# Kernel optimization log

Hardware: AMD Instinct MI355X
Metric: run time of the kernel (lower is better)

Reference implementation:

```python
import jax, jax.numpy as jnp
import numpy as np

N_NODES = 100000
N_EDGES = 3200000
IN_CH = 512
HIDDEN = 64
LOC_OUT = 16
OUT_CH = 40


def setup_inputs() -> dict:
    key = jax.random.key(0)
    ks = jax.random.split(key, 10)
    return {
        "batch_x": jax.random.normal(ks[0], (N_NODES, IN_CH), dtype=jnp.float32),
        "edge_index": jax.random.randint(ks[1], (2, N_EDGES), 0, N_NODES, dtype=jnp.int64),
        "glob_emb": jax.random.normal(ks[2], (N_NODES, LOC_OUT), dtype=jnp.float32),
        "W1": jax.random.normal(ks[3], (IN_CH, HIDDEN), dtype=jnp.float32) * (1.0 / np.sqrt(IN_CH)),
        "b1": jnp.zeros((HIDDEN,), dtype=jnp.float32),
        "W2": jax.random.normal(ks[4], (HIDDEN, LOC_OUT), dtype=jnp.float32) * (1.0 / np.sqrt(HIDDEN)),
        "b2": jnp.zeros((LOC_OUT,), dtype=jnp.float32),
        "att_w1": jax.random.normal(ks[5], (LOC_OUT, 16), dtype=jnp.float32) * 0.25,
        "att_b1": jnp.zeros((16,), dtype=jnp.float32),
        "att_w2": jax.random.normal(ks[6], (16, 1), dtype=jnp.float32) * 0.25,
        "lin1_w": jax.random.normal(ks[7], (LOC_OUT, OUT_CH), dtype=jnp.float32) * 0.25,
        "lin1_b": jnp.zeros((OUT_CH,), dtype=jnp.float32),
    }


def _gcn_conv(x, W, b, row, col, n):
    # GCNConv: out = D^-1/2 (A + I) D^-1/2 (X W) + b   (PyG default: self-loops, sym norm)
    h = x @ W
    loops = jnp.arange(n, dtype=row.dtype)
    row2 = jnp.concatenate([row, loops])  # sources (x_j)
    col2 = jnp.concatenate([col, loops])  # targets (aggregation index)
    deg = jax.ops.segment_sum(jnp.ones_like(col2, dtype=h.dtype), col2, num_segments=n)
    dinv = jax.lax.rsqrt(jnp.maximum(deg, 1.0))  # deg >= 1 thanks to self-loops
    norm = dinv[row2] * dinv[col2]               # [E+N]
    agg = jax.ops.segment_sum(h[row2] * norm[:, None], col2, num_segments=n)
    return agg + b


def reference(batch_x, edge_index, glob_emb, W1, b1, W2, b2, att_w1, att_b1, att_w2, lin1_w, lin1_b):
    n = batch_x.shape[0]
    row, col = edge_index[0], edge_index[1]
    x = _gcn_conv(batch_x, W1, b1, row, col, n)
    x = jax.nn.relu(x)  # dropout p=0.0 -> identity
    x = _gcn_conv(x, W2, b2, row, col, n)  # last layer: no relu/dropout
    z = jnp.stack([x, glob_emb], axis=1)  # [N, 2, 16]
    w = jnp.tanh(z @ att_w1 + att_b1) @ att_w2  # [N, 2, 1]
    beta = jax.nn.softmax(w, axis=1)
    emb = jnp.sum(beta * z, axis=1)  # [N, 16]
    return emb @ lin1_w + lin1_b  # [N, 40]
```

## Files before the change

kernel.cpp:

```cpp
#include <hip/hip_runtime.h>

#define N_IN 512
#define HID 64
#define NBLK 256

typedef __attribute__((ext_vector_type(4))) float f32x4;
typedef __attribute__((ext_vector_type(8))) short bf16x8;

__device__ inline float bf2f(unsigned short s) {
    union { unsigned int u; float f; } v; v.u = ((unsigned int)s) << 16; return v.f;
}
__device__ inline unsigned short f2bf(float f) {
    union { float f; unsigned int u; } v; v.f = f;
    unsigned int u = v.u;
    return (unsigned short)((u + 0x7FFFu + ((u >> 16) & 1u)) >> 16);
}

__global__ __launch_bounds__(1024) void k_histA_wt(const int* __restrict__ EI, int* __restrict__ hist,
                                                   const float* __restrict__ W1, unsigned short* __restrict__ Wt,
                                                   int E, int N, int K) {
    int tid = threadIdx.x;
    if (blockIdx.x >= NBLK) {
        int i = (blockIdx.x - NBLK) * 1024 + tid;
        if (i < N_IN * HID) {
            int k = i >> 6, n = i & 63;
            Wt[n * 512 + k] = f2bf(W1[i]);
        }
        return;
    }
    __shared__ int hs[512];
    __shared__ int sflag;
    if (tid == 0) sflag = (EI[1] == 0 && EI[3] == 0 && EI[5] == 0 && EI[7] == 0) ? 1 : 0;
    if (tid < 512) hs[tid] = 0;
    __syncthreads();
    bool f = sflag != 0;
    int chunk = (E + NBLK - 1) / NBLK;
    int s = blockIdx.x * chunk, e = min(E, s + chunk);
    for (int i = s + tid; i < e; i += 1024) {
        int c = f ? ((const int2*)EI)[E + i].x : EI[E + i];
        if ((unsigned)c < (unsigned)N) atomicAdd(&hs[c >> 8], 1);
    }
    __syncthreads();
    for (int k = tid; k < K; k += 1024) hist[k * NBLK + blockIdx.x] = hs[k];
}

__global__ __launch_bounds__(256) void k_scan_a2(int* __restrict__ data, int* __restrict__ bsum, int n) {
    __shared__ int sd[256];
    int i = blockIdx.x * 256 + threadIdx.x;
    int v = (i < n) ? data[i] : 0;
    sd[threadIdx.x] = v;
    __syncthreads();
    for (int off = 1; off < 256; off <<= 1) {
        int t = 0;
        if (threadIdx.x >= (unsigned)off) t = sd[threadIdx.x - off];
        __syncthreads();
        sd[threadIdx.x] += t;
        __syncthreads();
    }
    if (i < n) data[i] = sd[threadIdx.x] - v;
    if (threadIdx.x == 255) bsum[blockIdx.x] = sd[255];
}

__global__ __launch_bounds__(512) void k_scan_b(const int* __restrict__ bsum, int* __restrict__ bexc, int nb) {
    __shared__ int sd[512];
    int t = threadIdx.x;
    int v = (t < nb) ? bsum[t] : 0;
    sd[t] = v;
    __syncthreads();
    for (int off = 1; off < 512; off <<= 1) {
        int u = 0;
        if (t >= off) u = sd[t - off];
        __syncthreads();
        sd[t] += u;
        __syncthreads();
    }
    if (t < nb) bexc[t] = sd[t] - v;
    if (t == 511) bexc[nb] = sd[511];
}

__global__ __launch_bounds__(1024) void k_partB(const int* __restrict__ EI, const int* __restrict__ hist,
                                                const int* __restrict__ bexc, int* __restrict__ edges2,
                                                int E, int N, int K) {
    __shared__ int cur[512];
    __shared__ int sflag;
    int tid = threadIdx.x, b = blockIdx.x;
    if (tid == 0) sflag = (EI[1] == 0 && EI[3] == 0 && EI[5] == 0 && EI[7] == 0) ? 1 : 0;
    if (tid < 512) cur[tid] = (tid < K) ? (bexc[tid] + hist[tid * NBLK + b]) : 0;
    __syncthreads();
    bool f = sflag != 0;
    int chunk = (E + NBLK - 1) / NBLK;
    int s = b * chunk, e = min(E, s + chunk);
    for (int i = s + tid; i < e; i += 1024) {
        int r, c;
        if (f) { const int2* E2 = (const int2*)EI; r = E2[i].x; c = E2[E + i].x; }
        else   { r = EI[i]; c = EI[E + i]; }
        if ((unsigned)r >= (unsigned)N || (unsigned)c >= (unsigned)N) continue;
        int pos = atomicAdd(&cur[c >> 8], 1);
        edges2[pos] = r | ((c & 255) << 20);
    }
}

__global__ __launch_bounds__(256) void k_gemm1(const float* __restrict__ X, const unsigned short* __restrict__ Wt,
                                               unsigned short* __restrict__ H, int N) {
    int tid = threadIdx.x;
    int w = tid >> 6, lane = tid & 63;
    int m_l = lane & 15, q = lane >> 4;
    int m0 = blockIdx.x * 128 + w * 32;
    int rA0 = m0 + m_l, rA1 = m0 + 16 + m_l;
    int rc0 = rA0 < N ? rA0 : N - 1;
    int rc1 = rA1 < N ? rA1 : N - 1;
    const float* baseA0 = X + (size_t)rc0 * 512 + q * 8;
    const float* baseA1 = X + (size_t)rc1 * 512 + q * 8;
    const unsigned short* baseB = Wt + (size_t)m_l * 512 + q * 8;

    f32x4 acc[2][4] = {};
#pragma unroll 4
    for (int c = 0; c < 16; ++c) {
        int ko = c * 32;
        float4 x0a = *(const float4*)(baseA0 + ko);
        float4 x0b = *(const float4*)(baseA0 + ko + 4);
        float4 x1a = *(const float4*)(baseA1 + ko);
        float4 x1b = *(const float4*)(baseA1 + ko + 4);
        bf16x8 a0, a1;
        a0[0] = (short)f2bf(x0a.x); a0[1] = (short)f2bf(x0a.y); a0[2] = (short)f2bf(x0a.z); a0[3] = (short)f2bf(x0a.w);
        a0[4] = (short)f2bf(x0b.x); a0[5] = (short)f2bf(x0b.y); a0[6] = (short)f2bf(x0b.z); a0[7] = (short)f2bf(x0b.w);
        a1[0] = (short)f2bf(x1a.x); a1[1] = (short)f2bf(x1a.y); a1[2] = (short)f2bf(x1a.z); a1[3] = (short)f2bf(x1a.w);
        a1[4] = (short)f2bf(x1b.x); a1[5] = (short)f2bf(x1b.y); a1[6] = (short)f2bf(x1b.z); a1[7] = (short)f2bf(x1b.w);
#pragma unroll
        for (int t = 0; t < 4; ++t) {
            bf16x8 bb = *(const bf16x8*)(baseB + (size_t)t * 16 * 512 + ko);
            acc[0][t] = __builtin_amdgcn_mfma_f32_16x16x32_bf16(a0, bb, acc[0][t], 0, 0, 0);
            acc[1][t] = __builtin_amdgcn_mfma_f32_16x16x32_bf16(a1, bb, acc[1][t], 0, 0, 0);
        }
    }
#pragma unroll
    for (int h = 0; h < 2; ++h) {
#pragma unroll
        for (int rg = 0; rg < 4; ++rg) {
            int row = m0 + h * 16 + q * 4 + rg;
            if (row < N) {
#pragma unroll
                for (int t = 0; t < 4; ++t)
                    H[(size_t)row * 64 + t * 16 + m_l] = f2bf(acc[h][t][rg]);
            }
        }
    }
}

__global__ __launch_bounds__(256) void k_bucket(const int* __restrict__ bexc, const int* __restrict__ edges2,
                                                int* __restrict__ edges, int* __restrict__ start,
                                                float* __restrict__ dinv, unsigned short* __restrict__ H,
                                                int N, int K) {
    __shared__ int hist[256], sd[256], cur[256];
    __shared__ float dvs[256];
    int b = blockIdx.x, tid = threadIdx.x;
    int base = bexc[b];
    int end  = bexc[b + 1];
    hist[tid] = 0;
    __syncthreads();
    for (int i = base + tid; i < end; i += 256)
        atomicAdd(&hist[(edges2[i] >> 20) & 255], 1);
    __syncthreads();
    int v = hist[tid];
    sd[tid] = v;
    __syncthreads();
    for (int off = 1; off < 256; off <<= 1) {
        int t = 0;
        if (tid >= off) t = sd[tid - off];
        __syncthreads();
        sd[tid] += t;
        __syncthreads();
    }
    int excl = sd[tid] - v;
    cur[tid] = excl;
    int node = b * 256 + tid;
    float dvv = rsqrtf((float)(v + 1));
    dvs[tid] = dvv;
    if (node < N) {
        start[node] = base + excl;
        dinv[node] = dvv;
    }
    if (b == 0 && tid == 0) start[N] = bexc[K];
    __syncthreads();
    for (int i = base + tid; i < end; i += 256) {
        int pv = edges2[i];
        int pos = atomicAdd(&cur[(pv >> 20) & 255], 1);
        edges[base + pos] = pv & 0xFFFFF;
    }
    for (int rr = tid >> 4; rr < 256; rr += 16) {
        int n2 = b * 256 + rr;
        if (n2 < N) {
            float dv2 = dvs[rr];
            uint2* pp = (uint2*)(H + (size_t)n2 * 64 + (size_t)(tid & 15) * 4);
            uint2 vv = *pp;
            float f0 = bf2f((unsigned short)(vv.x & 0xffffu)) * dv2;
            float f1 = bf2f((unsigned short)(vv.x >> 16)) * dv2;
            float f2 = bf2f((unsigned short)(vv.y & 0xffffu)) * dv2;
            float f3 = bf2f((unsigned short)(vv.y >> 16)) * dv2;
            vv.x = (unsigned int)f2bf(f0) | ((unsigned int)f2bf(f1) << 16);
            vv.y = (unsigned int)f2bf(f2) | ((unsigned int)f2bf(f3) << 16);
            *pp = vv;
        }
    }
}

__global__ __launch_bounds__(256) void k_agg1g2(const unsigned short* __restrict__ H, const int* __restrict__ edges,
                                                const int* __restrict__ start, const float* __restrict__ dinv,
                                                const float* __restrict__ b1, const float* __restrict__ W2,
                                                unsigned short* __restrict__ H2, int N) {
    __shared__ float w2s[64 * 17];
    int tid = threadIdx.x;
    for (int i = tid; i < 1024; i += 256) { int k = i >> 4, c = i & 15; w2s[k * 17 + c] = W2[i]; }
    __syncthreads();
    int wid = blockIdx.x * 4 + (tid >> 6);
    int lane = tid & 63;
    if (wid >= N) return;
    int g = lane >> 4;
    int c4 = lane & 15;
    const size_t coff = (size_t)c4 * 4;
    float a0 = 0.f, a1 = 0.f, a2 = 0.f, a3 = 0.f;
    int s = start[wid], e = start[wid + 1];
    int i = s;
    if ((i & 3) && i < e) {
        int lim = min(e, (i + 3) & ~3);
        int j = i + g;
        if (j < lim) {
            uint2 v = *(const uint2*)(H + (size_t)edges[j] * 64 + coff);
            a0 += __uint_as_float(v.x << 16);
            a1 += __uint_as_float(v.x & 0xffff0000u);
            a2 += __uint_as_float(v.y << 16);
            a3 += __uint_as_float(v.y & 0xffff0000u);
        }
        i = lim;
    }
    for (; i + 32 <= e; i += 32) {
        int4 s0 = *(const int4*)(edges + i + g * 4);
        int4 s1 = *(const int4*)(edges + i + 16 + g * 4);
        uint2 v0 = *(const uint2*)(H + (size_t)s0.x * 64 + coff);
        uint2 v1 = *(const uint2*)(H + (size_t)s0.y * 64 + coff);
        uint2 v2 = *(const uint2*)(H + (size_t)s0.z * 64 + coff);
        uint2 v3 = *(const uint2*)(H + (size_t)s0.w * 64 + coff);
        uint2 v4 = *(const uint2*)(H + (size_t)s1.x * 64 + coff);
        uint2 v5 = *(const uint2*)(H + (size_t)s1.y * 64 + coff);
        uint2 v6 = *(const uint2*)(H + (size_t)s1.z * 64 + coff);
        uint2 v7 = *(const uint2*)(H + (size_t)s1.w * 64 + coff);
        a0 += __uint_as_float(v0.x << 16) + __uint_as_float(v1.x << 16)
            + __uint_as_float(v2.x << 16) + __uint_as_float(v3.x << 16)
            + __uint_as_float(v4.x << 16) + __uint_as_float(v5.x << 16)
            + __uint_as_float(v6.x << 16) + __uint_as_float(v7.x << 16);
        a1 += __uint_as_float(v0.x & 0xffff0000u) + __uint_as_float(v1.x & 0xffff0000u)
            + __uint_as_float(v2.x & 0xffff0000u) + __uint_as_float(v3.x & 0xffff0000u)
            + __uint_as_float(v4.x & 0xffff0000u) + __uint_as_float(v5.x & 0xffff0000u)
            + __uint_as_float(v6.x & 0xffff0000u) + __uint_as_float(v7.x & 0xffff0000u);
        a2 += __uint_as_float(v0.y << 16) + __uint_as_float(v1.y << 16)
            + __uint_as_float(v2.y << 16) + __uint_as_float(v3.y << 16)
            + __uint_as_float(v4.y << 16) + __uint_as_float(v5.y << 16)
            + __uint_as_float(v6.y << 16) + __uint_as_float(v7.y << 16);
        a3 += __uint_as_float(v0.y & 0xffff0000u) + __uint_as_float(v1.y & 0xffff0000u)
            + __uint_as_float(v2.y & 0xffff0000u) + __uint_as_float(v3.y & 0xffff0000u)
            + __uint_as_float(v4.y & 0xffff0000u) + __uint_as_float(v5.y & 0xffff0000u)
            + __uint_as_float(v6.y & 0xffff0000u) + __uint_as_float(v7.y & 0xffff0000u);
    }
    if (i + 16 <= e) {
        int4 sv = *(const int4*)(edges + i + g * 4);
        uint2 v0 = *(const uint2*)(H + (size_t)sv.x * 64 + coff);
        uint2 v1 = *(const uint2*)(H + (size_t)sv.y * 64 + coff);
        uint2 v2 = *(const uint2*)(H + (size_t)sv.z * 64 + coff);
        uint2 v3 = *(const uint2*)(H + (size_t)sv.w * 64 + coff);
        a0 += __uint_as_float(v0.x << 16) + __uint_as_float(v1.x << 16)
            + __uint_as_float(v2.x << 16) + __uint_as_float(v3.x << 16);
        a1 += __uint_as_float(v0.x & 0xffff0000u) + __uint_as_float(v1.x & 0xffff0000u)
            + __uint_as_float(v2.x & 0xffff0000u) + __uint_as_float(v3.x & 0xffff0000u);
        a2 += __uint_as_float(v0.y << 16) + __uint_as_float(v1.y << 16)
            + __uint_as_float(v2.y << 16) + __uint_as_float(v3.y << 16);
        a3 += __uint_as_float(v0.y & 0xffff0000u) + __uint_as_float(v1.y & 0xffff0000u)
            + __uint_as_float(v2.y & 0xffff0000u) + __uint_as_float(v3.y & 0xffff0000u);
        i += 16;
    }
    for (; i < e; i += 4) {
        int j = i + g;
        if (j < e) {
            uint2 v = *(const uint2*)(H + (size_t)edges[j] * 64 + coff);
            a0 += __uint_as_float(v.x << 16);
            a1 += __uint_as_float(v.x & 0xffff0000u);
            a2 += __uint_as_float(v.y << 16);
            a3 += __uint_as_float(v.y & 0xffff0000u);
        }
    }
    a0 += __shfl_xor(a0, 16, 64); a0 += __shfl_xor(a0, 32, 64);
    a1 += __shfl_xor(a1, 16, 64); a1 += __shfl_xor(a1, 32, 64);
    a2 += __shfl_xor(a2, 16, 64); a2 += __shfl_xor(a2, 32, 64);
    a3 += __shfl_xor(a3, 16, 64); a3 += __shfl_xor(a3, 32, 64);
    float dv = dinv[wid];
    uint2 sv = *(const uint2*)(H + (size_t)wid * 64 + coff);
    a0 += __uint_as_float(sv.x << 16);
    a1 += __uint_as_float(sv.x & 0xffff0000u);
    a2 += __uint_as_float(sv.y << 16);
    a3 += __uint_as_float(sv.y & 0xffff0000u);
    float4 bv = *(const float4*)(b1 + c4 * 4);
    float r0 = fmaxf(a0 * dv + bv.x, 0.f);
    float r1 = fmaxf(a1 * dv + bv.y, 0.f);
    float r2 = fmaxf(a2 * dv + bv.z, 0.f);
    float r3 = fmaxf(a3 * dv + bv.w, 0.f);
    float p = 0.f;
#pragma unroll
    for (int j = 0; j < 4; ++j) {
        int src = 4 * g + j;
        float x0 = __shfl(r0, src, 64);
        float x1 = __shfl(r1, src, 64);
        float x2 = __shfl(r2, src, 64);
        float x3 = __shfl(r3, src, 64);
        int kb = 16 * g + 4 * j;
        p += x0 * w2s[(kb + 0) * 17 + c4];
        p += x1 * w2s[(kb + 1) * 17 + c4];
        p += x2 * w2s[(kb + 2) * 17 + c4];
        p += x3 * w2s[(kb + 3) * 17 + c4];
    }
    p += __shfl_xor(p, 16, 64);
    p += __shfl_xor(p, 32, 64);
    if (g == 0) H2[(size_t)wid * 16 + c4] = f2bf(p * dv);
}

__global__ __launch_bounds__(256) void k_agg2(const unsigned short* __restrict__ H2, const int* __restrict__ edges,
                                              const int* __restrict__ start, const float* __restrict__ dinv,
                                              const float* __restrict__ b2, float* __restrict__ X2, int N) {
    int wid = blockIdx.x * 4 + (threadIdx.x >> 6);
    int lane = threadIdx.x & 63;
    if (wid >= N) return;
    int g = lane >> 3;
    int c2 = lane & 7;
    const size_t coff = (size_t)c2 * 2;
    float a0 = 0.f, a1 = 0.f;
    int s = start[wid], e = start[wid + 1];
    int i = s;
    if ((i & 3) && i < e) {
        int lim = min(e, (i + 3) & ~3);
        int j = i + g;
        if (j < lim) {
            unsigned int v = *(const unsigned int*)(H2 + (size_t)edges[j] * 16 + coff);
            a0 += __uint_as_float(v << 16);
            a1 += __uint_as_float(v & 0xffff0000u);
        }
        i = lim;
    }
    for (; i + 64 <= e; i += 64) {
        int4 s0 = *(const int4*)(edges + i + g * 4);
        int4 s1 = *(const int4*)(edges + i + 32 + g * 4);
        unsigned int v0 = *(const unsigned int*)(H2 + (size_t)s0.x * 16 + coff);
        unsigned int v1 = *(const unsigned int*)(H2 + (size_t)s0.y * 16 + coff);
        unsigned int v2 = *(const unsigned int*)(H2 + (size_t)s0.z * 16 + coff);
        unsigned int v3 = *(const unsigned int*)(H2 + (size_t)s0.w * 16 + coff);
        unsigned int v4 = *(const unsigned int*)(H2 + (size_t)s1.x * 16 + coff);
        unsigned int v5 = *(const unsigned int*)(H2 + (size_t)s1.y * 16 + coff);
        unsigned int v6 = *(const unsigned int*)(H2 + (size_t)s1.z * 16 + coff);
        unsigned int v7 = *(const unsigned int*)(H2 + (size_t)s1.w * 16 + coff);
        a0 += __uint_as_float(v0 << 16) + __uint_as_float(v1 << 16)
            + __uint_as_float(v2 << 16) + __uint_as_float(v3 << 16)
            + __uint_as_float(v4 << 16) + __uint_as_float(v5 << 16)
            + __uint_as_float(v6 << 16) + __uint_as_float(v7 << 16);
        a1 += __uint_as_float(v0 & 0xffff0000u) + __uint_as_float(v1 & 0xffff0000u)
            + __uint_as_float(v2 & 0xffff0000u) + __uint_as_float(v3 & 0xffff0000u)
            + __uint_as_float(v4 & 0xffff0000u) + __uint_as_float(v5 & 0xffff0000u)
            + __uint_as_float(v6 & 0xffff0000u) + __uint_as_float(v7 & 0xffff0000u);
    }
    if (i + 32 <= e) {
        int4 sv = *(const int4*)(edges + i + g * 4);
        unsigned int v0 = *(const unsigned int*)(H2 + (size_t)sv.x * 16 + coff);
        unsigned int v1 = *(const unsigned int*)(H2 + (size_t)sv.y * 16 + coff);
        unsigned int v2 = *(const unsigned int*)(H2 + (size_t)sv.z * 16 + coff);
        unsigned int v3 = *(const unsigned int*)(H2 + (size_t)sv.w * 16 + coff);
        a0 += __uint_as_float(v0 << 16) + __uint_as_float(v1 << 16)
            + __uint_as_float(v2 << 16) + __uint_as_float(v3 << 16);
        a1 += __uint_as_float(v0 & 0xffff0000u) + __uint_as_float(v1 & 0xffff0000u)
            + __uint_as_float(v2 & 0xffff0000u) + __uint_as_float(v3 & 0xffff0000u);
        i += 32;
    }
    for (; i < e; i += 8) {
        int j = i + g;
        if (j < e) {
            unsigned int v = *(const unsigned int*)(H2 + (size_t)edges[j] * 16 + coff);
            a0 += __uint_as_float(v << 16);
            a1 += __uint_as_float(v & 0xffff0000u);
        }
    }
    a0 += __shfl_xor(a0, 8, 64); a0 += __shfl_xor(a0, 16, 64); a0 += __shfl_xor(a0, 32, 64);
    a1 += __shfl_xor(a1, 8, 64); a1 += __shfl_xor(a1, 16, 64); a1 += __shfl_xor(a1, 32, 64);
    if (g == 0) {
        float dv = dinv[wid];
        unsigned int sv = *(const unsigned int*)(H2 + (size_t)wid * 16 + coff);
        a0 += __uint_as_float(sv << 16);
        a1 += __uint_as_float(sv & 0xffff0000u);
        float2 bv = *(const float2*)(b2 + c2 * 2);
        float2 o; o.x = a0 * dv + bv.x; o.y = a1 * dv + bv.y;
        *(float2*)(X2 + (size_t)wid * 16 + coff) = o;
    }
}

__global__ __launch_bounds__(256) void k_head(const float* __restrict__ X2, const float* __restrict__ G,
                                              const float* __restrict__ AW1, const float* __restrict__ AB1,
                                              const float* __restrict__ AW2, const float* __restrict__ LW,
                                              const float* __restrict__ LB, float* __restrict__ OUT, int N) {
    __shared__ float s_aw1[256], s_ab1[16], s_aw2[16], s_lw[640], s_lb[40];
    int tid = threadIdx.x;
    s_aw1[tid] = AW1[tid];
    if (tid < 16) { s_ab1[tid] = AB1[tid]; s_aw2[tid] = AW2[tid]; }
    for (int i = tid; i < 640; i += 256) s_lw[i] = LW[i];
    if (tid < 40) s_lb[tid] = LB[tid];
    __syncthreads();
    int node = blockIdx.x * 256 + tid;
    if (node >= N) return;
    float x[16], g[16];
    const float4* xp = (const float4*)(X2 + (size_t)node * 16);
    const float4* gp = (const float4*)(G + (size_t)node * 16);
#pragma unroll
    for (int q = 0; q < 4; ++q) {
        float4 v = xp[q]; x[q*4] = v.x; x[q*4+1] = v.y; x[q*4+2] = v.z; x[q*4+3] = v.w;
        float4 u = gp[q]; g[q*4] = u.x; g[q*4+1] = u.y; g[q*4+2] = u.z; g[q*4+3] = u.w;
    }
    float wx = 0.f, wg = 0.f;
#pragma unroll
    for (int j = 0; j < 16; ++j) {
        float tx = s_ab1[j], tg = s_ab1[j];
#pragma unroll
        for (int c = 0; c < 16; ++c) { tx += x[c] * s_aw1[c*16 + j]; tg += g[c] * s_aw1[c*16 + j]; }
        wx += tanhf(tx) * s_aw2[j];
        wg += tanhf(tg) * s_aw2[j];
    }
    float m = fmaxf(wx, wg);
    float ex = expf(wx - m), eg = expf(wg - m);
    float inv = 1.f / (ex + eg);
    float bx = ex * inv, bg = eg * inv;
    float emb[16];
#pragma unroll
    for (int c = 0; c < 16; ++c) emb[c] = bx * x[c] + bg * g[c];
    float* op = OUT + (size_t)node * 40;
    for (int o = 0; o < 40; ++o) {
        float a = s_lb[o];
#pragma unroll
        for (int c = 0; c < 16; ++c) a += emb[c] * s_lw[c*40 + o];
        op[o] = a;
    }
}

extern "C" void kernel_launch(void* const* d_in, const int* in_sizes, int n_in,
                              void* d_out, int out_size, void* d_ws, size_t ws_size,
                              hipStream_t stream) {
    const float* X   = (const float*)d_in[0];
    const int*   EI  = (const int*)d_in[1];
    const float* G   = (const float*)d_in[2];
    const float* W1  = (const float*)d_in[3];
    const float* B1  = (const float*)d_in[4];
    const float* W2  = (const float*)d_in[5];
    const float* B2  = (const float*)d_in[6];
    const float* AW1 = (const float*)d_in[7];
    const float* AB1 = (const float*)d_in[8];
    const float* AW2 = (const float*)d_in[9];
    const float* LW  = (const float*)d_in[10];
    const float* LB  = (const float*)d_in[11];
    float* OUT = (float*)d_out;

    const int N = in_sizes[0] / N_IN;
    const int E = in_sizes[1] / 2;
    const int NB = (N + 255) / 256;
    const int K  = NB;
    const int NH = K * NBLK;
    const int SB = (NH + 255) / 256;
    const int WB = (N_IN * HID + 1023) / 1024;
    const int GB = (N + 127) / 128;

    char* w = (char*)d_ws;
    size_t off = 0;
    auto take = [&](size_t bytes) -> void* {
        void* p = (void*)(w + off);
        off = (off + bytes + 255) & ~(size_t)255;
        return p;
    };
    int*   hist   = (int*)take((size_t)NH * 4);
    int*   bsum   = (int*)take((size_t)SB * 4);
    int*   bexc   = (int*)take((size_t)(SB + 1) * 4);
    int*   startp = (int*)take((size_t)(N + 1) * 4);
    float* dinvp  = (float*)take((size_t)N * 4);
    int*   edges2 = (int*)take((size_t)E * 4);
    int*   edges  = (int*)take((size_t)E * 4);
    unsigned short* wt = (unsigned short*)take((size_t)N_IN * HID * 2);
    unsigned short* h1 = (unsigned short*)take((size_t)N * 64 * 2);
    unsigned short* h2 = (unsigned short*)take((size_t)N * 16 * 2);
    float* x2 = (float*)take((size_t)N * 16 * 4);
    (void)ws_size; (void)n_in; (void)out_size;

    k_histA_wt<<<NBLK + WB, 1024, 0, stream>>>(EI, hist, W1, wt, E, N, K);
    k_scan_a2 <<<SB, 256, 0, stream>>>(hist, bsum, NH);
    k_scan_b  <<<1, 512, 0, stream>>>(bsum, bexc, SB);
    k_partB   <<<NBLK, 1024, 0, stream>>>(EI, hist, bexc, edges2, E, N, K);
    k_gemm1   <<<GB, 256, 0, stream>>>(X, wt, h1, N);
    k_bucket  <<<K, 256, 0, stream>>>(bexc, edges2, edges, startp, dinvp, h1, N, K);
    k_agg1g2  <<<(N + 3) / 4, 256, 0, stream>>>(h1, edges, startp, dinvp, B1, W2, h2, N);
    k_agg2    <<<(N + 3) / 4, 256, 0, stream>>>(h2, edges, startp, dinvp, B2, x2, N);
    k_head    <<<NB, 256, 0, stream>>>(x2, G, AW1, AB1, AW2, LW, LB, OUT, N);
}
```

Measured before the change: 575.2 us.

## Split layer-1 aggregation into four column-slab passes for cache locality

```diff
diff --git a/kernel.cpp b/kernel.cpp
--- a/kernel.cpp
+++ b/kernel.cpp
@@ -141,7 +141,7 @@
             if (row < N) {
 #pragma unroll
                 for (int t = 0; t < 4; ++t)
-                    H[(size_t)row * 64 + t * 16 + m_l] = f2bf(acc[h][t][rg]);
+                    H[((size_t)t * N + row) * 16 + m_l] = f2bf(acc[h][t][rg]);
             }
         }
     }
@@ -187,138 +187,123 @@
         int pos = atomicAdd(&cur[(pv >> 20) & 255], 1);
         edges[base + pos] = pv & 0xFFFFF;
     }
-    for (int rr = tid >> 4; rr < 256; rr += 16) {
-        int n2 = b * 256 + rr;
-        if (n2 < N) {
-            float dv2 = dvs[rr];
-            uint2* pp = (uint2*)(H + (size_t)n2 * 64 + (size_t)(tid & 15) * 4);
-            uint2 vv = *pp;
-            float f0 = bf2f((unsigned short)(vv.x & 0xffffu)) * dv2;
-            float f1 = bf2f((unsigned short)(vv.x >> 16)) * dv2;
-            float f2 = bf2f((unsigned short)(vv.y & 0xffffu)) * dv2;
-            float f3 = bf2f((unsigned short)(vv.y >> 16)) * dv2;
-            vv.x = (unsigned int)f2bf(f0) | ((unsigned int)f2bf(f1) << 16);
-            vv.y = (unsigned int)f2bf(f2) | ((unsigned int)f2bf(f3) << 16);
-            *pp = vv;
-        }
-    }
-}
-
-__global__ __launch_bounds__(256) void k_agg1g2(const unsigned short* __restrict__ H, const int* __restrict__ edges,
-                                                const int* __restrict__ start, const float* __restrict__ dinv,
-                                                const float* __restrict__ b1, const float* __restrict__ W2,
-                                                unsigned short* __restrict__ H2, int N) {
-    __shared__ float w2s[64 * 17];
-    int tid = threadIdx.x;
-    for (int i = tid; i < 1024; i += 256) { int k = i >> 4, c = i & 15; w2s[k * 17 + c] = W2[i]; }
-    __syncthreads();
-    int wid = blockIdx.x * 4 + (tid >> 6);
-    int lane = tid & 63;
+#pragma unroll
+    for (int p = 0; p < 4; ++p) {
+        for (int i = tid; i < 256 * 8; i += 256) {
+            int rr = i >> 3, q = i & 7;
+            int n2 = b * 256 + rr;
+            if (n2 < N) {
+                float dv2 = dvs[rr];
+                unsigned int* pp = (unsigned int*)(H + ((size_t)p * N + n2) * 16 + q * 2);
+                unsigned int vv = *pp;
+                float f0 = bf2f((unsigned short)(vv & 0xffffu)) * dv2;
+                float f1 = bf2f((unsigned short)(vv >> 16)) * dv2;
+                *pp = (unsigned int)f2bf(f0) | ((unsigned int)f2bf(f1) << 16);
+            }
+        }
+    }
+}
+
+__global__ __launch_bounds__(256) void k_agg1p(const unsigned short* __restrict__ H, const int* __restrict__ edges,
+                                               const int* __restrict__ start, const float* __restrict__ dinv,
+                                               const float* __restrict__ b1, float* __restrict__ x1f,
+                                               int N, int p) {
+    int wid = blockIdx.x * 4 + (threadIdx.x >> 6);
+    int lane = threadIdx.x & 63;
     if (wid >= N) return;
-    int g = lane >> 4;
-    int c4 = lane & 15;
-    const size_t coff = (size_t)c4 * 4;
-    float a0 = 0.f, a1 = 0.f, a2 = 0.f, a3 = 0.f;
+    const unsigned short* Hp = H + (size_t)p * N * 16;
+    int g = lane >> 3;
+    int c2 = lane & 7;
+    const size_t coff = (size_t)c2 * 2;
+    float a0 = 0.f, a1 = 0.f;
     int s = start[wid], e = start[wid + 1];
     int i = s;
     if ((i & 3) && i < e) {
         int lim = min(e, (i + 3) & ~3);
         int j = i + g;
         if (j < lim) {
-            uint2 v = *(const uint2*)(H + (size_t)edges[j] * 64 + coff);
-            a0 += __uint_as_float(v.x << 16);
-            a1 += __uint_as_float(v.x & 0xffff0000u);
-            a2 += __uint_as_float(v.y << 16);
-            a3 += __uint_as_float(v.y & 0xffff0000u);
+            unsigned int v = *(const unsigned int*)(Hp + (size_t)edges[j] * 16 + coff);
+            a0 += __uint_as_float(v << 16);
+            a1 += __uint_as_float(v & 0xffff0000u);
         }
         i = lim;
     }
-    for (; i + 32 <= e; i += 32) {
+    for (; i + 64 <= e; i += 64) {
         int4 s0 = *(const int4*)(edges + i + g * 4);
-        int4 s1 = *(const int4*)(edges + i + 16 + g * 4);
-        uint2 v0 = *(const uint2*)(H + (size_t)s0.x * 64 + coff);
-        uint2 v1 = *(const uint2*)(H + (size_t)s0.y * 64 + coff);
-        uint2 v2 = *(const uint2*)(H + (size_t)s0.z * 64 + coff);
-        uint2 v3 = *(const uint2*)(H + (size_t)s0.w * 64 + coff);
-        uint2 v4 = *(const uint2*)(H + (size_t)s1.x * 64 + coff);
-        uint2 v5 = *(const uint2*)(H + (size_t)s1.y * 64 + coff);
-        uint2 v6 = *(const uint2*)(H + (size_t)s1.z * 64 + coff);
-        uint2 v7 = *(const uint2*)(H + (size_t)s1.w * 64 + coff);
-        a0 += __uint_as_float(v0.x << 16) + __uint_as_float(v1.x << 16)
-            + __uint_as_float(v2.x << 16) + __uint_as_float(v3.x << 16)
-            + __uint_as_float(v4.x << 16) + __uint_as_float(v5.x << 16)
-            + __uint_as_float(v6.x << 16) + __uint_as_float(v7.x << 16);
-        a1 += __uint_as_float(v0.x & 0xffff0000u) + __uint_as_float(v1.x & 0xffff0000u)
-            + __uint_as_float(v2.x & 0xffff0000u) + __uint_as_float(v3.x & 0xffff0000u)
-            + __uint_as_float(v4.x & 0xffff0000u) + __uint_as_float(v5.x & 0xffff0000u)
-            + __uint_as_float(v6.x & 0xffff0000u) + __uint_as_float(v7.x & 0xffff0000u);
-        a2 += __uint_as_float(v0.y << 16) + __uint_as_float(v1.y << 16)
-            + __uint_as_float(v2.y << 16) + __uint_as_float(v3.y << 16)
-            + __uint_as_float(v4.y << 16) + __uint_as_float(v5.y << 16)
-            + __uint_as_float(v6.y << 16) + __uint_as_float(v7.y << 16);
-        a3 += __uint_as_float(v0.y & 0xffff0000u) + __uint_as_float(v1.y & 0xffff0000u)
-            + __uint_as_float(v2.y & 0xffff0000u) + __uint_as_float(v3.y & 0xffff0000u)
-            + __uint_as_float(v4.y & 0xffff0000u) + __uint_as_float(v5.y & 0xffff0000u)
-            + __uint_as_float(v6.y & 0xffff0000u) + __uint_as_float(v7.y & 0xffff0000u);
-    }
-    if (i + 16 <= e) {
+        int4 s1 = *(const int4*)(edges + i + 32 + g * 4);
+        unsigned int v0 = *(const unsigned int*)(Hp + (size_t)s0.x * 16 + coff);
+        unsigned int v1 = *(const unsigned int*)(Hp + (size_t)s0.y * 16 + coff);
+        unsigned int v2 = *(const unsigned int*)(Hp + (size_t)s0.z * 16 + coff);
+        unsigned int v3 = *(const unsigned int*)(Hp + (size_t)s0.w * 16 + coff);
+        unsigned int v4 = *(const unsigned int*)(Hp + (size_t)s1.x * 16 + coff);
+        unsigned int v5 = *(const unsigned int*)(Hp + (size_t)s1.y * 16 + coff);
+        unsigned int v6 = *(const unsigned int*)(Hp + (size_t)s1.z * 16 + coff);
+        unsigned int v7 = *(const unsigned int*)(Hp + (size_t)s1.w * 16 + coff);
+        a0 += __uint_as_float(v0 << 16) + __uint_as_float(v1 << 16)
+            + __uint_as_float(v2 << 16) + __uint_as_float(v3 << 16)
+            + __uint_as_float(v4 << 16) + __uint_as_float(v5 << 16)
+            + __uint_as_float(v6 << 16) + __uint_as_float(v7 << 16);
+        a1 += __uint_as_float(v0 & 0xffff0000u) + __uint_as_float(v1 & 0xffff0000u)
+            + __uint_as_float(v2 & 0xffff0000u) + __uint_as_float(v3 & 0xffff0000u)
+            + __uint_as_float(v4 & 0xffff0000u) + __uint_as_float(v5 & 0xffff0000u)
+            + __uint_as_float(v6 & 0xffff0000u) + __uint_as_float(v7 & 0xffff0000u);
+    }
+    if (i + 32 <= e) {
         int4 sv = *(const int4*)(edges + i + g * 4);
-        uint2 v0 = *(const uint2*)(H + (size_t)sv.x * 64 + coff);
-        uint2 v1 = *(const uint2*)(H + (size_t)sv.y * 64 + coff);
-        uint2 v2 = *(const uint2*)(H + (size_t)sv.z * 64 + coff);
-        uint2 v3 = *(const uint2*)(H + (size_t)sv.w * 64 + coff);
-        a0 += __uint_as_float(v0.x << 16) + __uint_as_float(v1.x << 16)
-            + __uint_as_float(v2.x << 16) + __uint_as_float(v3.x << 16);
-        a1 += __uint_as_float(v0.x & 0xffff0000u) + __uint_as_float(v1.x & 0xffff0000u)
-            + __uint_as_float(v2.x & 0xffff0000u) + __uint_as_float(v3.x & 0xffff0000u);
-        a2 += __uint_as_float(v0.y << 16) + __uint_as_float(v1.y << 16)
-            + __uint_as_float(v2.y << 16) + __uint_as_float(v3.y << 16);
-        a3 += __uint_as_float(v0.y & 0xffff0000u) + __uint_as_float(v1.y & 0xffff0000u)
-            + __uint_as_float(v2.y & 0xffff0000u) + __uint_as_float(v3.y & 0xffff0000u);
-        i += 16;
-    }
-    for (; i < e; i += 4) {
+        unsigned int v0 = *(const unsigned int*)(Hp + (size_t)sv.x * 16 + coff);
+        unsigned int v1 = *(const unsigned int*)(Hp + (size_t)sv.y * 16 + coff);
+        unsigned int v2 = *(const unsigned int*)(Hp + (size_t)sv.z * 16 + coff);
+        unsigned int v3 = *(const unsigned int*)(Hp + (size_t)sv.w * 16 + coff);
+        a0 += __uint_as_float(v0 << 16) + __uint_as_float(v1 << 16)
+            + __uint_as_float(v2 << 16) + __uint_as_float(v3 << 16);
+        a1 += __uint_as_float(v0 & 0xffff0000u) + __uint_as_float(v1 & 0xffff0000u)
+            + __uint_as_float(v2 & 0xffff0000u) + __uint_as_float(v3 & 0xffff0000u);
+        i += 32;
+    }
+    for (; i < e; i += 8) {
         int j = i + g;
         if (j < e) {
-            uint2 v = *(const uint2*)(H + (size_t)edges[j] * 64 + coff);
-            a0 += __uint_as_float(v.x << 16);
-            a1 += __uint_as_float(v.x & 0xffff0000u);
-            a2 += __uint_as_float(v.y << 16);
-            a3 += __uint_as_float(v.y & 0xffff0000u);
-        }
-    }
-    a0 += __shfl_xor(a0, 16, 64); a0 += __shfl_xor(a0, 32, 64);
-    a1 += __shfl_xor(a1, 16, 64); a1 += __shfl_xor(a1, 32, 64);
-    a2 += __shfl_xor(a2, 16, 64); a2 += __shfl_xor(a2, 32, 64);
-    a3 += __shfl_xor(a3, 16, 64); a3 += __shfl_xor(a3, 32, 64);
-    float dv = dinv[wid];
-    uint2 sv = *(const uint2*)(H + (size_t)wid * 64 + coff);
-    a0 += __uint_as_float(sv.x << 16);
-    a1 += __uint_as_float(sv.x & 0xffff0000u);
-    a2 += __uint_as_float(sv.y << 16);
-    a3 += __uint_as_float(sv.y & 0xffff0000u);
-    float4 bv = *(const float4*)(b1 + c4 * 4);
-    float r0 = fmaxf(a0 * dv + bv.x, 0.f);
-    float r1 = fmaxf(a1 * dv + bv.y, 0.f);
-    float r2 = fmaxf(a2 * dv + bv.z, 0.f);
-    float r3 = fmaxf(a3 * dv + bv.w, 0.f);
-    float p = 0.f;
-#pragma unroll
-    for (int j = 0; j < 4; ++j) {
-        int src = 4 * g + j;
-        float x0 = __shfl(r0, src, 64);
-        float x1 = __shfl(r1, src, 64);
-        float x2 = __shfl(r2, src, 64);
-        float x3 = __shfl(r3, src, 64);
-        int kb = 16 * g + 4 * j;
-        p += x0 * w2s[(kb + 0) * 17 + c4];
-        p += x1 * w2s[(kb + 1) * 17 + c4];
-        p += x2 * w2s[(kb + 2) * 17 + c4];
-        p += x3 * w2s[(kb + 3) * 17 + c4];
-    }
-    p += __shfl_xor(p, 16, 64);
-    p += __shfl_xor(p, 32, 64);
-    if (g == 0) H2[(size_t)wid * 16 + c4] = f2bf(p * dv);
+            unsigned int v = *(const unsigned int*)(Hp + (size_t)edges[j] * 16 + coff);
+            a0 += __uint_as_float(v << 16);
+            a1 += __uint_as_float(v & 0xffff0000u);
+        }
+    }
+    a0 += __shfl_xor(a0, 8, 64); a0 += __shfl_xor(a0, 16, 64); a0 += __shfl_xor(a0, 32, 64);
+    a1 += __shfl_xor(a1, 8, 64); a1 += __shfl_xor(a1, 16, 64); a1 += __shfl_xor(a1, 32, 64);
+    if (g == 0) {
+        float dv = dinv[wid];
+        unsigned int sv = *(const unsigned int*)(Hp + (size_t)wid * 16 + coff);
+        a0 += __uint_as_float(sv << 16);
+        a1 += __uint_as_float(sv & 0xffff0000u);
+        float2 bv = *(const float2*)(b1 + p * 16 + c2 * 2);
+        float2 o;
+        o.x = fmaxf(a0 * dv + bv.x, 0.f);
+        o.y = fmaxf(a1 * dv + bv.y, 0.f);
+        *(float2*)(x1f + (size_t)wid * 64 + p * 16 + c2 * 2) = o;
+    }
+}
+
+__global__ __launch_bounds__(256) void k_gemm2v(const float* __restrict__ x1f, const float* __restrict__ W2,
+                                                const float* __restrict__ dinv, unsigned short* __restrict__ H2,
+                                                int N) {
+    __shared__ float w2s[64 * 17];
+    int tid = threadIdx.x;
+    for (int i = tid; i < 1024; i += 256) { int k = i >> 4, c = i & 15; w2s[k * 17 + c] = W2[i]; }
+    __syncthreads();
+    int t = blockIdx.x * 256 + tid;
+    int node = t >> 4, c = t & 15;
+    if (node >= N) return;
+    const float4* xp = (const float4*)(x1f + (size_t)node * 64);
+    float acc = 0.f;
+#pragma unroll
+    for (int kq = 0; kq < 16; ++kq) {
+        float4 v = xp[kq];
+        acc += v.x * w2s[(kq * 4 + 0) * 17 + c];
+        acc += v.y * w2s[(kq * 4 + 1) * 17 + c];
+        acc += v.z * w2s[(kq * 4 + 2) * 17 + c];
+        acc += v.w * w2s[(kq * 4 + 3) * 17 + c];
+    }
+    H2[(size_t)node * 16 + c] = f2bf(acc * dinv[node]);
 }
 
 __global__ __launch_bounds__(256) void k_agg2(const unsigned short* __restrict__ H2, const int* __restrict__ edges,
@@ -485,7 +470,8 @@
     unsigned short* wt = (unsigned short*)take((size_t)N_IN * HID * 2);
     unsigned short* h1 = (unsigned short*)take((size_t)N * 64 * 2);
     unsigned short* h2 = (unsigned short*)take((size_t)N * 16 * 2);
-    float* x2 = (float*)take((size_t)N * 16 * 4);
+    float* x1f = (float*)take((size_t)N * 64 * 4);
+    float* x2  = (float*)take((size_t)N * 16 * 4);
     (void)ws_size; (void)n_in; (void)out_size;
 
     k_histA_wt<<<NBLK + WB, 1024, 0, stream>>>(EI, hist, W1, wt, E, N, K);
@@ -494,7 +480,9 @@
     k_partB   <<<NBLK, 1024, 0, stream>>>(EI, hist, bexc, edges2, E, N, K);
     k_gemm1   <<<GB, 256, 0, stream>>>(X, wt, h1, N);
     k_bucket  <<<K, 256, 0, stream>>>(bexc, edges2, edges, startp, dinvp, h1, N, K);
-    k_agg1g2  <<<(N + 3) / 4, 256, 0, stream>>>(h1, edges, startp, dinvp, B1, W2, h2, N);
+    for (int p = 0; p < 4; ++p)
+        k_agg1p <<<(N + 3) / 4, 256, 0, stream>>>(h1, edges, startp, dinvp, B1, x1f, N, p);
+    k_gemm2v  <<<(N * 16 + 255) / 256, 256, 0, stream>>>(x1f, W2, dinvp, h2, N);
     k_agg2    <<<(N + 3) / 4, 256, 0, stream>>>(h2, edges, startp, dinvp, B2, x2, N);
     k_head    <<<NB, 256, 0, stream>>>(x2, G, AW1, AB1, AW2, LW, LB, OUT, N);
 }
```

Result: slower. 693.5 us (+20.6%).

## Pad CSR segments to 4-aligned starts and gather from a zero sentinel row

Applied to the files above, without the earlier changes.

```diff
diff --git a/kernel.cpp b/kernel.cpp
--- a/kernel.cpp
+++ b/kernel.cpp
@@ -61,9 +61,13 @@
     if (threadIdx.x == 255) bsum[blockIdx.x] = sd[255];
 }
 
-__global__ __launch_bounds__(512) void k_scan_b(const int* __restrict__ bsum, int* __restrict__ bexc, int nb) {
+__global__ __launch_bounds__(512) void k_scan_b(const int* __restrict__ bsum, int* __restrict__ bexc, int nb,
+                                                unsigned short* __restrict__ h1, unsigned short* __restrict__ h2,
+                                                int N) {
     __shared__ int sd[512];
     int t = threadIdx.x;
+    if (t < 32) ((unsigned int*)(h1 + (size_t)N * 64))[t] = 0;
+    if (t >= 32 && t < 40) ((unsigned int*)(h2 + (size_t)N * 16))[t - 32] = 0;
     int v = (t < nb) ? bsum[t] : 0;
     sd[t] = v;
     __syncthreads();
@@ -149,20 +153,22 @@
 
 __global__ __launch_bounds__(256) void k_bucket(const int* __restrict__ bexc, const int* __restrict__ edges2,
                                                 int* __restrict__ edges, int* __restrict__ start,
-                                                float* __restrict__ dinv, unsigned short* __restrict__ H,
-                                                int N, int K) {
+                                                int* __restrict__ endv, float* __restrict__ dinv,
+                                                unsigned short* __restrict__ H, int N, int K) {
     __shared__ int hist[256], sd[256], cur[256];
     __shared__ float dvs[256];
     int b = blockIdx.x, tid = threadIdx.x;
-    int base = bexc[b];
-    int end  = bexc[b + 1];
+    int cbase = bexc[b];
+    int cend  = bexc[b + 1];
+    int base  = ((cbase + 3) & ~3) + 1024 * b;
     hist[tid] = 0;
     __syncthreads();
-    for (int i = base + tid; i < end; i += 256)
+    for (int i = cbase + tid; i < cend; i += 256)
         atomicAdd(&hist[(edges2[i] >> 20) & 255], 1);
     __syncthreads();
     int v = hist[tid];
-    sd[tid] = v;
+    int v4 = (v + 3) & ~3;
+    sd[tid] = v4;
     __syncthreads();
     for (int off = 1; off < 256; off <<= 1) {
         int t = 0;
@@ -171,18 +177,18 @@
         sd[tid] += t;
         __syncthreads();
     }
-    int excl = sd[tid] - v;
+    int excl = sd[tid] - v4;
     cur[tid] = excl;
     int node = b * 256 + tid;
     float dvv = rsqrtf((float)(v + 1));
     dvs[tid] = dvv;
     if (node < N) {
         start[node] = base + excl;
-        dinv[node] = dvv;
-    }
-    if (b == 0 && tid == 0) start[N] = bexc[K];
-    __syncthreads();
-    for (int i = base + tid; i < end; i += 256) {
+        endv[node]  = base + excl + v;
+        dinv[node]  = dvv;
+    }
+    __syncthreads();
+    for (int i = cbase + tid; i < cend; i += 256) {
         int pv = edges2[i];
         int pos = atomicAdd(&cur[(pv >> 20) & 255], 1);
         edges[base + pos] = pv & 0xFFFFF;
@@ -205,7 +211,8 @@
 }
 
 __global__ __launch_bounds__(256) void k_agg1g2(const unsigned short* __restrict__ H, const int* __restrict__ edges,
-                                                const int* __restrict__ start, const float* __restrict__ dinv,
+                                                const int* __restrict__ start, const int* __restrict__ endv,
+                                                const float* __restrict__ dinv,
                                                 const float* __restrict__ b1, const float* __restrict__ W2,
                                                 unsigned short* __restrict__ H2, int N) {
     __shared__ float w2s[64 * 17];
@@ -219,31 +226,35 @@
     int c4 = lane & 15;
     const size_t coff = (size_t)c4 * 4;
     float a0 = 0.f, a1 = 0.f, a2 = 0.f, a3 = 0.f;
-    int s = start[wid], e = start[wid + 1];
-    int i = s;
-    if ((i & 3) && i < e) {
-        int lim = min(e, (i + 3) & ~3);
-        int j = i + g;
-        if (j < lim) {
-            uint2 v = *(const uint2*)(H + (size_t)edges[j] * 64 + coff);
-            a0 += __uint_as_float(v.x << 16);
-            a1 += __uint_as_float(v.x & 0xffff0000u);
-            a2 += __uint_as_float(v.y << 16);
-            a3 += __uint_as_float(v.y & 0xffff0000u);
-        }
-        i = lim;
-    }
-    for (; i + 32 <= e; i += 32) {
-        int4 s0 = *(const int4*)(edges + i + g * 4);
-        int4 s1 = *(const int4*)(edges + i + 16 + g * 4);
-        uint2 v0 = *(const uint2*)(H + (size_t)s0.x * 64 + coff);
-        uint2 v1 = *(const uint2*)(H + (size_t)s0.y * 64 + coff);
-        uint2 v2 = *(const uint2*)(H + (size_t)s0.z * 64 + coff);
-        uint2 v3 = *(const uint2*)(H + (size_t)s0.w * 64 + coff);
-        uint2 v4 = *(const uint2*)(H + (size_t)s1.x * 64 + coff);
-        uint2 v5 = *(const uint2*)(H + (size_t)s1.y * 64 + coff);
-        uint2 v6 = *(const uint2*)(H + (size_t)s1.z * 64 + coff);
-        uint2 v7 = *(const uint2*)(H + (size_t)s1.w * 64 + coff);
+    int s = start[wid], e = endv[wid];
+    int4 s0, s1;
+    if (s < e) {
+        s0 = *(const int4*)(edges + s + g * 4);
+        s1 = *(const int4*)(edges + s + 16 + g * 4);
+    }
+    for (int i = s; i < e; i += 32) {
+        int jb0 = i + g * 4, jb1 = i + 16 + g * 4;
+        int i0 = (jb0 + 0 < e) ? s0.x : N;
+        int i1 = (jb0 + 1 < e) ? s0.y : N;
+        int i2 = (jb0 + 2 < e) ? s0.z : N;
+        int i3 = (jb0 + 3 < e) ? s0.w : N;
+        int i4 = (jb1 + 0 < e) ? s1.x : N;
+        int i5 = (jb1 + 1 < e) ? s1.y : N;
+        int i6 = (jb1 + 2 < e) ? s1.z : N;
+        int i7 = (jb1 + 3 < e) ? s1.w : N;
+        uint2 v0 = *(const uint2*)(H + (size_t)i0 * 64 + coff);
+        uint2 v1 = *(const uint2*)(H + (size_t)i1 * 64 + coff);
+        uint2 v2 = *(const uint2*)(H + (size_t)i2 * 64 + coff);
+        uint2 v3 = *(const uint2*)(H + (size_t)i3 * 64 + coff);
+        uint2 v4 = *(const uint2*)(H + (size_t)i4 * 64 + coff);
+        uint2 v5 = *(const uint2*)(H + (size_t)i5 * 64 + coff);
+        uint2 v6 = *(const uint2*)(H + (size_t)i6 * 64 + coff);
+        uint2 v7 = *(const uint2*)(H + (size_t)i7 * 64 + coff);
+        int ni = i + 32;
+        if (ni < e) {
+            s0 = *(const int4*)(edges + ni + g * 4);
+            s1 = *(const int4*)(edges + ni + 16 + g * 4);
+        }
         a0 += __uint_as_float(v0.x << 16) + __uint_as_float(v1.x << 16)
             + __uint_as_float(v2.x << 16) + __uint_as_float(v3.x << 16)
             + __uint_as_float(v4.x << 16) + __uint_as_float(v5.x << 16)
@@ -261,32 +272,6 @@
             + __uint_as_float(v4.y & 0xffff0000u) + __uint_as_float(v5.y & 0xffff0000u)
             + __uint_as_float(v6.y & 0xffff0000u) + __uint_as_float(v7.y & 0xffff0000u);
     }
-    if (i + 16 <= e) {
-        int4 sv = *(const int4*)(edges + i + g * 4);
-        uint2 v0 = *(const uint2*)(H + (size_t)sv.x * 64 + coff);
-        uint2 v1 = *(const uint2*)(H + (size_t)sv.y * 64 + coff);
-        uint2 v2 = *(const uint2*)(H + (size_t)sv.z * 64 + coff);
-        uint2 v3 = *(const uint2*)(H + (size_t)sv.w * 64 + coff);
-        a0 += __uint_as_float(v0.x << 16) + __uint_as_float(v1.x << 16)
-            + __uint_as_float(v2.x << 16) + __uint_as_float(v3.x << 16);
-        a1 += __uint_as_float(v0.x & 0xffff0000u) + __uint_as_float(v1.x & 0xffff0000u)
-            + __uint_as_float(v2.x & 0xffff0000u) + __uint_as_float(v3.x & 0xffff0000u);
-        a2 += __uint_as_float(v0.y << 16) + __uint_as_float(v1.y << 16)
-            + __uint_as_float(v2.y << 16) + __uint_as_float(v3.y << 16);
-        a3 += __uint_as_float(v0.y & 0xffff0000u) + __uint_as_float(v1.y & 0xffff0000u)
-            + __uint_as_float(v2.y & 0xffff0000u) + __uint_as_float(v3.y & 0xffff0000u);
-        i += 16;
-    }
-    for (; i < e; i += 4) {
-        int j = i + g;
-        if (j < e) {
-            uint2 v = *(const uint2*)(H + (size_t)edges[j] * 64 + coff);
-            a0 += __uint_as_float(v.x << 16);
-            a1 += __uint_as_float(v.x & 0xffff0000u);
-            a2 += __uint_as_float(v.y << 16);
-            a3 += __uint_as_float(v.y & 0xffff0000u);
-        }
-    }
     a0 += __shfl_xor(a0, 16, 64); a0 += __shfl_xor(a0, 32, 64);
     a1 += __shfl_xor(a1, 16, 64); a1 += __shfl_xor(a1, 32, 64);
     a2 += __shfl_xor(a2, 16, 64); a2 += __shfl_xor(a2, 32, 64);
@@ -322,7 +307,8 @@
 }
 
 __global__ __launch_bounds__(256) void k_agg2(const unsigned short* __restrict__ H2, const int* __restrict__ edges,
-                                              const int* __restrict__ start, const float* __restrict__ dinv,
+                                              const int* __restrict__ start, const int* __restrict__ endv,
+                                              const float* __restrict__ dinv,
                                               const float* __restrict__ b2, float* __restrict__ X2, int N) {
     int wid = blockIdx.x * 4 + (threadIdx.x >> 6);
     int lane = threadIdx.x & 63;
@@ -331,29 +317,35 @@
     int c2 = lane & 7;
     const size_t coff = (size_t)c2 * 2;
     float a0 = 0.f, a1 = 0.f;
-    int s = start[wid], e = start[wid + 1];
-    int i = s;
-    if ((i & 3) && i < e) {
-        int lim = min(e, (i + 3) & ~3);
-        int j = i + g;
-        if (j < lim) {
-            unsigned int v = *(const unsigned int*)(H2 + (size_t)edges[j] * 16 + coff);
-            a0 += __uint_as_float(v << 16);
-            a1 += __uint_as_float(v & 0xffff0000u);
-        }
-        i = lim;
-    }
-    for (; i + 64 <= e; i += 64) {
-        int4 s0 = *(const int4*)(edges + i + g * 4);
-        int4 s1 = *(const int4*)(edges + i + 32 + g * 4);
-        unsigned int v0 = *(const unsigned int*)(H2 + (size_t)s0.x * 16 + coff);
-        unsigned int v1 = *(const unsigned int*)(H2 + (size_t)s0.y * 16 + coff);
-        unsigned int v2 = *(const unsigned int*)(H2 + (size_t)s0.z * 16 + coff);
-        unsigned int v3 = *(const unsigned int*)(H2 + (size_t)s0.w * 16 + coff);
-        unsigned int v4 = *(const unsigned int*)(H2 + (size_t)s1.x * 16 + coff);
-        unsigned int v5 = *(const unsigned int*)(H2 + (size_t)s1.y * 16 + coff);
-        unsigned int v6 = *(const unsigned int*)(H2 + (size_t)s1.z * 16 + coff);
-        unsigned int v7 = *(const unsigned int*)(H2 + (size_t)s1.w * 16 + coff);
+    int s = start[wid], e = endv[wid];
+    int4 s0, s1;
+    if (s < e) {
+        s0 = *(const int4*)(edges + s + g * 4);
+        s1 = *(const int4*)(edges + s + 32 + g * 4);
+    }
+    for (int i = s; i < e; i += 64) {
+        int jb0 = i + g * 4, jb1 = i + 32 + g * 4;
+        int i0 = (jb0 + 0 < e) ? s0.x : N;
+        int i1 = (jb0 + 1 < e) ? s0.y : N;
+        int i2 = (jb0 + 2 < e) ? s0.z : N;
+        int i3 = (jb0 + 3 < e) ? s0.w : N;
+        int i4 = (jb1 + 0 < e) ? s1.x : N;
+        int i5 = (jb1 + 1 < e) ? s1.y : N;
+        int i6 = (jb1 + 2 < e) ? s1.z : N;
+        int i7 = (jb1 + 3 < e) ? s1.w : N;
+        unsigned int v0 = *(const unsigned int*)(H2 + (size_t)i0 * 16 + coff);
+        unsigned int v1 = *(const unsigned int*)(H2 + (size_t)i1 * 16 + coff);
+        unsigned int v2 = *(const unsigned int*)(H2 + (size_t)i2 * 16 + coff);
+        unsigned int v3 = *(const unsigned int*)(H2 + (size_t)i3 * 16 + coff);
+        unsigned int v4 = *(const unsigned int*)(H2 + (size_t)i4 * 16 + coff);
+        unsigned int v5 = *(const unsigned int*)(H2 + (size_t)i5 * 16 + coff);
+        unsigned int v6 = *(const unsigned int*)(H2 + (size_t)i6 * 16 + coff);
+        unsigned int v7 = *(const unsigned int*)(H2 + (size_t)i7 * 16 + coff);
+        int ni = i + 64;
+        if (ni < e) {
+            s0 = *(const int4*)(edges + ni + g * 4);
+            s1 = *(const int4*)(edges + ni + 32 + g * 4);
+        }
         a0 += __uint_as_float(v0 << 16) + __uint_as_float(v1 << 16)
             + __uint_as_float(v2 << 16) + __uint_as_float(v3 << 16)
             + __uint_as_float(v4 << 16) + __uint_as_float(v5 << 16)
@@ -362,26 +354,6 @@
             + __uint_as_float(v2 & 0xffff0000u) + __uint_as_float(v3 & 0xffff0000u)
             + __uint_as_float(v4 & 0xffff0000u) + __uint_as_float(v5 & 0xffff0000u)
             + __uint_as_float(v6 & 0xffff0000u) + __uint_as_float(v7 & 0xffff0000u);
-    }
-    if (i + 32 <= e) {
-        int4 sv = *(const int4*)(edges + i + g * 4);
-        unsigned int v0 = *(const unsigned int*)(H2 + (size_t)sv.x * 16 + coff);
-        unsigned int v1 = *(const unsigned int*)(H2 + (size_t)sv.y * 16 + coff);
-        unsigned int v2 = *(const unsigned int*)(H2 + (size_t)sv.z * 16 + coff);
-        unsigned int v3 = *(const unsigned int*)(H2 + (size_t)sv.w * 16 + coff);
-        a0 += __uint_as_float(v0 << 16) + __uint_as_float(v1 << 16)
-            + __uint_as_float(v2 << 16) + __uint_as_float(v3 << 16);
-        a1 += __uint_as_float(v0 & 0xffff0000u) + __uint_as_float(v1 & 0xffff0000u)
-            + __uint_as_float(v2 & 0xffff0000u) + __uint_as_float(v3 & 0xffff0000u);
-        i += 32;
-    }
-    for (; i < e; i += 8) {
-        int j = i + g;
-        if (j < e) {
-            unsigned int v = *(const unsigned int*)(H2 + (size_t)edges[j] * 16 + coff);
-            a0 += __uint_as_float(v << 16);
-            a1 += __uint_as_float(v & 0xffff0000u);
-        }
     }
     a0 += __shfl_xor(a0, 8, 64); a0 += __shfl_xor(a0, 16, 64); a0 += __shfl_xor(a0, 32, 64);
     a1 += __shfl_xor(a1, 8, 64); a1 += __shfl_xor(a1, 16, 64); a1 += __shfl_xor(a1, 32, 64);
@@ -478,23 +450,24 @@
     int*   hist   = (int*)take((size_t)NH * 4);
     int*   bsum   = (int*)take((size_t)SB * 4);
     int*   bexc   = (int*)take((size_t)(SB + 1) * 4);
-    int*   startp = (int*)take((size_t)(N + 1) * 4);
+    int*   startp = (int*)take((size_t)N * 4);
+    int*   endp   = (int*)take((size_t)N * 4);
     float* dinvp  = (float*)take((size_t)N * 4);
     int*   edges2 = (int*)take((size_t)E * 4);
-    int*   edges  = (int*)take((size_t)E * 4);
+    int*   edges  = (int*)take((size_t)(E + 1024 * (size_t)K + 256) * 4);
     unsigned short* wt = (unsigned short*)take((size_t)N_IN * HID * 2);
-    unsigned short* h1 = (unsigned short*)take((size_t)N * 64 * 2);
-    unsigned short* h2 = (unsigned short*)take((size_t)N * 16 * 2);
+    unsigned short* h1 = (unsigned short*)take((size_t)(N + 1) * 64 * 2);
+    unsigned short* h2 = (unsigned short*)take((size_t)(N + 1) * 16 * 2);
     float* x2 = (float*)take((size_t)N * 16 * 4);
     (void)ws_size; (void)n_in; (void)out_size;
 
     k_histA_wt<<<NBLK + WB, 1024, 0, stream>>>(EI, hist, W1, wt, E, N, K);
     k_scan_a2 <<<SB, 256, 0, stream>>>(hist, bsum, NH);
-    k_scan_b  <<<1, 512, 0, stream>>>(bsum, bexc, SB);
+    k_scan_b  <<<1, 512, 0, stream>>>(bsum, bexc, SB, h1, h2, N);
     k_partB   <<<NBLK, 1024, 0, stream>>>(EI, hist, bexc, edges2, E, N, K);
     k_gemm1   <<<GB, 256, 0, stream>>>(X, wt, h1, N);
-    k_bucket  <<<K, 256, 0, stream>>>(bexc, edges2, edges, startp, dinvp, h1, N, K);
-    k_agg1g2  <<<(N + 3) / 4, 256, 0, stream>>>(h1, edges, startp, dinvp, B1, W2, h2, N);
-    k_agg2    <<<(N + 3) / 4, 256, 0, stream>>>(h2, edges, startp, dinvp, B2, x2, N);
+    k_bucket  <<<K, 256, 0, stream>>>(bexc, edges2, edges, startp, endp, dinvp, h1, N, K);
+    k_agg1g2  <<<(N + 3) / 4, 256, 0, stream>>>(h1, edges, startp, endp, dinvp, B1, W2, h2, N);
+    k_agg2    <<<(N + 3) / 4, 256, 0, stream>>>(h2, edges, startp, endp, dinvp, B2, x2, N);
     k_head    <<<NB, 256, 0, stream>>>(x2, G, AW1, AB1, AW2, LW, LB, OUT, N);
 }
```

New measurement: 531.4 us. 1.08x faster.
